# Optimization experiments

Measured on AMD Instinct MI355X. Metric: run time of the kernel, lower is better.

## Reference

```python
import jax, jax.numpy as jnp
import numpy as np

B, C, H = 8, 768, 12
TH = TW = 16
SH = SW = 32
N = TH * TW + SH * SW  # 1280


def setup_inputs() -> dict:
    key = jax.random.key(0)
    k1, k2, k3 = jax.random.split(key, 3)
    return {
        "x": jax.random.normal(k1, (B, N, C), jnp.float32),
        "qkv_w": jax.random.normal(k2, (3 * C, C), jnp.float32) * 0.02,
        "proj_w": jax.random.normal(k3, (C, C), jnp.float32) * 0.02,
        "proj_b": jnp.zeros((C,), jnp.float32),
        "t_h": TH, "t_w": TW, "s_h": SH, "s_w": SW,
    }


def reference(x, qkv_w, proj_w, proj_b, t_h, t_w, s_h, s_w):
    Bb, Nn, Cc = x.shape
    hd = Cc // H
    scale = hd ** -0.5
    nt = t_h * t_w
    ns = s_h * s_w
    # qkv projection: torch Linear computes x @ W.T
    qkv = (x @ qkv_w.T).reshape(Bb, Nn, 3, H, hd).transpose(2, 0, 3, 1, 4)
    q, k, v = qkv[0], qkv[1], qkv[2]  # each [B, H, N, hd]
    q_mt, q_s = q[:, :, :nt], q[:, :, nt:]
    k_mt, v_mt = k[:, :, :nt], v[:, :, :nt]
    # template queries attend only to template keys
    attn_t = jax.nn.softmax(jnp.einsum('bhqd,bhkd->bhqk', q_mt, k_mt) * scale, axis=-1)
    x_mt = jnp.einsum('bhqk,bhkd->bhqd', attn_t, v_mt).transpose(0, 2, 1, 3).reshape(Bb, nt, Cc)
    # search queries attend to all (template + search) keys
    attn_s = jax.nn.softmax(jnp.einsum('bhqd,bhkd->bhqk', q_s, k) * scale, axis=-1)
    x_s = jnp.einsum('bhqk,bhkd->bhqd', attn_s, v).transpose(0, 2, 1, 3).reshape(Bb, ns, Cc)
    out = jnp.concatenate([x_mt, x_s], axis=1)
    out = out @ proj_w.T + proj_b
    return out
```

## Files before the change

### kernel.cpp

```cpp
#include <hip/hip_runtime.h>


typedef __attribute__((ext_vector_type(8))) short s8v;
typedef __attribute__((ext_vector_type(4))) float f4v;
typedef __attribute__((ext_vector_type(4))) unsigned short u4v;

#define MFMA16(a, b, c) __builtin_amdgcn_mfma_f32_16x16x32_bf16((a), (b), (c), 0, 0, 0)

#define QSCALE 0.1803368801f

__device__ __forceinline__ unsigned short f2bf(float f) {
  unsigned int u = __builtin_bit_cast(unsigned int, f);
  u += 0x7fffu + ((u >> 16) & 1u);
  return (unsigned short)(u >> 16);
}

__global__ __launch_bounds__(256) void cvt_kernel(const float* __restrict__ src,
                                                  unsigned short* __restrict__ dst,
                                                  int n4) {
  int i = blockIdx.x * 256 + threadIdx.x;
  if (i < n4) {
    f4v v = ((const f4v*)src)[i];
    u4v o;
    o[0] = f2bf(v[0]); o[1] = f2bf(v[1]); o[2] = f2bf(v[2]); o[3] = f2bf(v[3]);
    ((u4v*)dst)[i] = o;
  }
}

__global__ __launch_bounds__(256) void gemm_qkv_kernel(
    const unsigned short* __restrict__ A,
    const unsigned short* __restrict__ Bm,
    unsigned short* __restrict__ qb, unsigned short* __restrict__ kb,
    unsigned short* __restrict__ vT) {
  const int K = 768;
  __shared__ __align__(16) unsigned short As[128 * 32];
  __shared__ __align__(16) unsigned short Bs[128 * 32];
  int tid = threadIdx.x;
  int wave = tid >> 6, lane = tid & 63;
  int quad = lane >> 4, l16 = lane & 15;
  int wm = wave >> 1, wn = wave & 1;
  int m0 = blockIdx.y * 128, n0 = blockIdx.x * 128;

  f4v acc[4][4];
#pragma unroll
  for (int i = 0; i < 4; ++i)
#pragma unroll
    for (int j = 0; j < 4; ++j) acc[i][j] = (f4v){0.f, 0.f, 0.f, 0.f};

  for (int kt = 0; kt < K; kt += 32) {
#pragma unroll
    for (int c = 0; c < 2; ++c) {
      int idx = c * 256 + tid;
      int row = idx >> 2;
      int col = (idx & 3) << 3;
      const unsigned short* ga = A + (size_t)(m0 + row) * K + (kt + col);
      const unsigned short* gb = Bm + (size_t)(n0 + row) * K + (kt + col);
      __builtin_amdgcn_global_load_lds(
          (const __attribute__((address_space(1))) unsigned int*)ga,
          (__attribute__((address_space(3))) unsigned int*)((char*)As + idx * 16), 16, 0, 0);
      __builtin_amdgcn_global_load_lds(
          (const __attribute__((address_space(1))) unsigned int*)gb,
          (__attribute__((address_space(3))) unsigned int*)((char*)Bs + idx * 16), 16, 0, 0);
    }
    __syncthreads();
    s8v af[4], bfr[4];
#pragma unroll
    for (int mi = 0; mi < 4; ++mi)
      af[mi] = *(const s8v*)&As[(wm * 64 + mi * 16 + l16) * 32 + quad * 8];
#pragma unroll
    for (int ni = 0; ni < 4; ++ni)
      bfr[ni] = *(const s8v*)&Bs[(wn * 64 + ni * 16 + l16) * 32 + quad * 8];
#pragma unroll
    for (int mi = 0; mi < 4; ++mi)
#pragma unroll
      for (int ni = 0; ni < 4; ++ni)
        acc[mi][ni] = MFMA16(af[mi], bfr[ni], acc[mi][ni]);
    __syncthreads();
  }

#pragma unroll
  for (int ni = 0; ni < 4; ++ni) {
    int gn = n0 + wn * 64 + ni * 16 + l16;
    int which = gn / 768;
    int oo = gn - which * 768;
    int hh = oo >> 6;
    int dd = oo & 63;
#pragma unroll
    for (int mi = 0; mi < 4; ++mi) {
#pragma unroll
      for (int r = 0; r < 4; ++r) {
        int gm = m0 + wm * 64 + mi * 16 + quad * 4 + r;
        int bb = gm / 1280;
        int nn = gm - bb * 1280;
        float v = acc[mi][ni][r];
        if (which == 0) {
          qb[(((size_t)bb * 12 + hh) * 1280 + nn) * 64 + dd] = f2bf(v * QSCALE);
        } else if (which == 1) {
          kb[(((size_t)bb * 12 + hh) * 1280 + nn) * 64 + dd] = f2bf(v);
        } else {
          vT[(((size_t)bb * 12 + hh) * 64 + dd) * 1280 + nn] = f2bf(v);
        }
      }
    }
  }
}

__global__ __launch_bounds__(256) void gemm_proj_kernel(
    const unsigned short* __restrict__ A,
    const unsigned short* __restrict__ Bm,
    const float* __restrict__ pb, float* __restrict__ out) {
  const int K = 768;
  __shared__ __align__(16) unsigned short As[128 * 32];
  __shared__ __align__(16) unsigned short Bs[128 * 32];
  int tid = threadIdx.x;
  int wave = tid >> 6, lane = tid & 63;
  int quad = lane >> 4, l16 = lane & 15;
  int wm = wave >> 1, wn = wave & 1;
  int m0 = blockIdx.y * 128, n0 = blockIdx.x * 128;

  f4v acc[4][4];
#pragma unroll
  for (int i = 0; i < 4; ++i)
#pragma unroll
    for (int j = 0; j < 4; ++j) acc[i][j] = (f4v){0.f, 0.f, 0.f, 0.f};

  for (int kt = 0; kt < K; kt += 32) {
#pragma unroll
    for (int c = 0; c < 2; ++c) {
      int idx = c * 256 + tid;
      int row = idx >> 2;
      int col = (idx & 3) << 3;
      const unsigned short* ga = A + (size_t)(m0 + row) * K + (kt + col);
      const unsigned short* gb = Bm + (size_t)(n0 + row) * K + (kt + col);
      __builtin_amdgcn_global_load_lds(
          (const __attribute__((address_space(1))) unsigned int*)ga,
          (__attribute__((address_space(3))) unsigned int*)((char*)As + idx * 16), 16, 0, 0);
      __builtin_amdgcn_global_load_lds(
          (const __attribute__((address_space(1))) unsigned int*)gb,
          (__attribute__((address_space(3))) unsigned int*)((char*)Bs + idx * 16), 16, 0, 0);
    }
    __syncthreads();
    s8v af[4], bfr[4];
#pragma unroll
    for (int mi = 0; mi < 4; ++mi)
      af[mi] = *(const s8v*)&As[(wm * 64 + mi * 16 + l16) * 32 + quad * 8];
#pragma unroll
    for (int ni = 0; ni < 4; ++ni)
      bfr[ni] = *(const s8v*)&Bs[(wn * 64 + ni * 16 + l16) * 32 + quad * 8];
#pragma unroll
    for (int mi = 0; mi < 4; ++mi)
#pragma unroll
      for (int ni = 0; ni < 4; ++ni)
        acc[mi][ni] = MFMA16(af[mi], bfr[ni], acc[mi][ni]);
    __syncthreads();
  }

#pragma unroll
  for (int ni = 0; ni < 4; ++ni) {
    int gn = n0 + wn * 64 + ni * 16 + l16;
    float bias = pb[gn];
#pragma unroll
    for (int mi = 0; mi < 4; ++mi)
#pragma unroll
      for (int r = 0; r < 4; ++r) {
        int gm = m0 + wm * 64 + mi * 16 + quad * 4 + r;
        out[(size_t)gm * 768 + gn] = acc[mi][ni][r] + bias;
      }
  }
}

__global__ __launch_bounds__(256) void attn_kernel(
    const unsigned short* __restrict__ qb, const unsigned short* __restrict__ kb,
    const unsigned short* __restrict__ vT, unsigned short* __restrict__ attnb) {
  const int NT = 1280, CC = 768;
  int bx = blockIdx.x;
  int qt = (bx < 16) ? (bx + 4) : (bx - 16);
  int h = blockIdx.y;
  int b = blockIdx.z;
  int wave = threadIdx.x >> 6, lane = threadIdx.x & 63;
  int quad = lane >> 4, l16 = lane & 15;
  int q0 = qt * 64 + wave * 16;
  int nk = (qt < 4) ? 256 : 1280;
  int ntiles = nk >> 6;

  const unsigned short* qp = qb + (((size_t)b * 12 + h) * NT + q0) * 64;
  const unsigned short* kp = kb + (((size_t)b * 12 + h) * NT) * 64;
  const unsigned short* vp = vT + (((size_t)b * 12 + h) * 64) * NT;

  __shared__ __align__(16) unsigned short Kl[2][8][512];
  __shared__ __align__(16) unsigned short Vl[2][8][512];

  s8v bq0 = *(const s8v*)(qp + l16 * 64 + quad * 8);
  s8v bq1 = *(const s8v*)(qp + l16 * 64 + 32 + quad * 8);

  int perm = ((l16 >> 2) << 3) + (l16 & 3);
  int f0 = wave * 2, f1 = wave * 2 + 1;
  int koffs0, koffs1, voffs0, voffs1;
  {
    int s = f0 >> 2, dh = (f0 >> 1) & 1, hh = f0 & 1;
    koffs0 = (s * 32 + hh * 4 + perm) * 64 + (dh * 4 + quad) * 8;
    s = f1 >> 2; dh = (f1 >> 1) & 1; hh = f1 & 1;
    koffs1 = (s * 32 + hh * 4 + perm) * 64 + (dh * 4 + quad) * 8;
    int dt = f0 >> 1, sv = f0 & 1;
    voffs0 = (dt * 16 + l16) * NT + sv * 32 + quad * 8;
    dt = f1 >> 1; sv = f1 & 1;
    voffs1 = (dt * 16 + l16) * NT + sv * 32 + quad * 8;
  }

#define STAGE(bfi, k0_)                                                                     \
  do {                                                                                      \
    __builtin_amdgcn_global_load_lds(                                                       \
        (const __attribute__((address_space(1))) unsigned int*)(kp + (size_t)(k0_)*64 +     \
                                                                koffs0),                    \
        (__attribute__((address_space(3))) unsigned int*)((char*)&Kl[bfi][f0][0] +          \
                                                          lane * 16),                       \
        16, 0, 0);                                                                          \
    __builtin_amdgcn_global_load_lds(                                                       \
        (const __attribute__((address_space(1))) unsigned int*)(kp + (size_t)(k0_)*64 +     \
                                                                koffs1),                    \
        (__attribute__((address_space(3))) unsigned int*)((char*)&Kl[bfi][f1][0] +          \
                                                          lane * 16),                       \
        16, 0, 0);                                                                          \
    __builtin_amdgcn_global_load_lds(                                                       \
        (const __attribute__((address_space(1))) unsigned int*)(vp + (size_t)(k0_) +        \
                                                                voffs0),                    \
        (__attribute__((address_space(3))) unsigned int*)((char*)&Vl[bfi][f0][0] +          \
                                                          lane * 16),                       \
        16, 0, 0);                                                                          \
    __builtin_amdgcn_global_load_lds(                                                       \
        (const __attribute__((address_space(1))) unsigned int*)(vp + (size_t)(k0_) +        \
                                                                voffs1),                    \
        (__attribute__((address_space(3))) unsigned int*)((char*)&Vl[bfi][f1][0] +          \
                                                          lane * 16),                       \
        16, 0, 0);                                                                          \
  } while (0)

  float l_part = 0.f;
  f4v Oacc[4];
#pragma unroll
  for (int dt = 0; dt < 4; ++dt) Oacc[dt] = (f4v){0.f, 0.f, 0.f, 0.f};

  STAGE(0, 0);

  for (int t = 0; t < ntiles; ++t) {
    __syncthreads();
    int bf = t & 1;
    if (t + 1 < ntiles) STAGE(bf ^ 1, (t + 1) * 64);

    s8v kf[8], vf[8];
#pragma unroll
    for (int f = 0; f < 8; ++f) kf[f] = *(const s8v*)&Kl[bf][f][lane * 8];
#pragma unroll
    for (int g = 0; g < 8; ++g) vf[g] = *(const s8v*)&Vl[bf][g][lane * 8];

#pragma unroll
    for (int s = 0; s < 2; ++s) {
      f4v s0 = {0.f, 0.f, 0.f, 0.f}, s1 = {0.f, 0.f, 0.f, 0.f};
      s0 = MFMA16(kf[(s << 2) | 0], bq0, s0);
      s0 = MFMA16(kf[(s << 2) | 2], bq1, s0);
      s1 = MFMA16(kf[(s << 2) | 1], bq0, s1);
      s1 = MFMA16(kf[(s << 2) | 3], bq1, s1);

      float p0[4], p1[4];
#pragma unroll
      for (int r = 0; r < 4; ++r) {
        p0[r] = __builtin_amdgcn_exp2f(s0[r]);
        p1[r] = __builtin_amdgcn_exp2f(s1[r]);
      }
      l_part += ((p0[0] + p0[1]) + (p0[2] + p0[3])) + ((p1[0] + p1[1]) + (p1[2] + p1[3]));

      s8v pbf;
#pragma unroll
      for (int r = 0; r < 4; ++r) {
        pbf[r] = (short)f2bf(p0[r]);
        pbf[4 + r] = (short)f2bf(p1[r]);
      }

#pragma unroll
      for (int dt = 0; dt < 4; ++dt) Oacc[dt] = MFMA16(vf[dt * 2 + s], pbf, Oacc[dt]);
    }
  }
#undef STAGE

  float l = l_part;
  l += __shfl_xor(l, 16, 64);
  l += __shfl_xor(l, 32, 64);
  float inv = 1.f / l;

  size_t orow = ((size_t)b * NT + q0 + l16) * CC + h * 64;
#pragma unroll
  for (int dt = 0; dt < 4; ++dt) {
    u4v ov;
#pragma unroll
    for (int r = 0; r < 4; ++r) ov[r] = f2bf(Oacc[dt][r] * inv);
    *(u4v*)(attnb + orow + dt * 16 + quad * 4) = ov;
  }
}

extern "C" void kernel_launch(void* const* d_in, const int* in_sizes, int n_in,
                              void* d_out, int out_size, void* d_ws, size_t ws_size,
                              hipStream_t stream) {
  const float* x = (const float*)d_in[0];
  const float* qkv_w = (const float*)d_in[1];
  const float* proj_w = (const float*)d_in[2];
  const float* proj_b = (const float*)d_in[3];
  float* out = (float*)d_out;

  char* ws = (char*)d_ws;
  unsigned short* xb = (unsigned short*)(ws + 0);
  unsigned short* wqkvb = (unsigned short*)(ws + 15728640);
  unsigned short* wpb = (unsigned short*)(ws + 19267584);
  unsigned short* qb = (unsigned short*)(ws + 20447232);
  unsigned short* kbuf = (unsigned short*)(ws + 36175872);
  unsigned short* vT = (unsigned short*)(ws + 51904512);
  unsigned short* attnb = xb;

  cvt_kernel<<<dim3(1966080 / 256), 256, 0, stream>>>(x, xb, 1966080);
  cvt_kernel<<<dim3(442368 / 256), 256, 0, stream>>>(qkv_w, wqkvb, 442368);
  cvt_kernel<<<dim3(576), 256, 0, stream>>>(proj_w, wpb, 147456);

  gemm_qkv_kernel<<<dim3(18, 80), 256, 0, stream>>>(xb, wqkvb, qb, kbuf, vT);
  attn_kernel<<<dim3(20, 12, 8), 256, 0, stream>>>(qb, kbuf, vT, attnb);
  gemm_proj_kernel<<<dim3(6, 80), 256, 0, stream>>>(attnb, wpb, proj_b, out);
}
```

Measured before the change: 285.2 us.

## Process 32 queries per wave in attention to reuse K/V tiles; fuse conversions

Each attention wave now handles two 16-row query blocks (128 queries per block), so every K/V fragment loaded from LDS feeds twice as many MFMAs and the grid is halved. The probability packing uses the packed bf16 conversion intrinsic, and the three fp32-to-bf16 conversion launches become one kernel. In exchange, register pressure per wave rises and there are fewer blocks to keep the GPU busy.

```diff
diff --git a/kernel.cpp b/kernel.cpp
--- a/kernel.cpp
+++ b/kernel.cpp
@@ -1,9 +1,11 @@
 #include <hip/hip_runtime.h>
+#include <hip/hip_bf16.h>
 
 
 typedef __attribute__((ext_vector_type(8))) short s8v;
 typedef __attribute__((ext_vector_type(4))) float f4v;
 typedef __attribute__((ext_vector_type(4))) unsigned short u4v;
+typedef __attribute__((ext_vector_type(4))) unsigned int u4i;
 
 #define MFMA16(a, b, c) __builtin_amdgcn_mfma_f32_16x16x32_bf16((a), (b), (c), 0, 0, 0)
 
@@ -15,16 +17,43 @@
   return (unsigned short)(u >> 16);
 }
 
-__global__ __launch_bounds__(256) void cvt_kernel(const float* __restrict__ src,
-                                                  unsigned short* __restrict__ dst,
-                                                  int n4) {
+__device__ __forceinline__ unsigned int pk2(float lo, float hi) {
+  __hip_bfloat162 t = __float22bfloat162_rn(make_float2(lo, hi));
+  unsigned int u;
+  __builtin_memcpy(&u, &t, 4);
+  return u;
+}
+
+__device__ __forceinline__ s8v pack8(const float* p0, const float* p1) {
+  u4i pi;
+  pi[0] = pk2(p0[0], p0[1]);
+  pi[1] = pk2(p0[2], p0[3]);
+  pi[2] = pk2(p1[0], p1[1]);
+  pi[3] = pk2(p1[2], p1[3]);
+  return __builtin_bit_cast(s8v, pi);
+}
+
+__global__ __launch_bounds__(256) void cvt3_kernel(const float* __restrict__ x,
+                                                   const float* __restrict__ wq,
+                                                   const float* __restrict__ wp,
+                                                   unsigned short* __restrict__ xb,
+                                                   unsigned short* __restrict__ wqb,
+                                                   unsigned short* __restrict__ wpb) {
   int i = blockIdx.x * 256 + threadIdx.x;
-  if (i < n4) {
-    f4v v = ((const f4v*)src)[i];
-    u4v o;
-    o[0] = f2bf(v[0]); o[1] = f2bf(v[1]); o[2] = f2bf(v[2]); o[3] = f2bf(v[3]);
-    ((u4v*)dst)[i] = o;
-  }
+  const float* src;
+  unsigned short* dst;
+  int j;
+  if (i < 1966080) {
+    src = x; dst = xb; j = i;
+  } else if (i < 1966080 + 442368) {
+    src = wq; dst = wqb; j = i - 1966080;
+  } else {
+    src = wp; dst = wpb; j = i - (1966080 + 442368);
+  }
+  f4v v = ((const f4v*)src)[j];
+  u4v o;
+  o[0] = f2bf(v[0]); o[1] = f2bf(v[1]); o[2] = f2bf(v[2]); o[3] = f2bf(v[3]);
+  ((u4v*)dst)[j] = o;
 }
 
 __global__ __launch_bounds__(256) void gemm_qkv_kernel(
@@ -174,16 +203,17 @@
     const unsigned short* __restrict__ vT, unsigned short* __restrict__ attnb) {
   const int NT = 1280, CC = 768;
   int bx = blockIdx.x;
-  int qt = (bx < 16) ? (bx + 4) : (bx - 16);
   int h = blockIdx.y;
   int b = blockIdx.z;
+  int nk, qstart;
+  if (bx < 8) { nk = 1280; qstart = 256 + bx * 128; }
+  else        { nk = 256;  qstart = (bx - 8) * 128; }
   int wave = threadIdx.x >> 6, lane = threadIdx.x & 63;
   int quad = lane >> 4, l16 = lane & 15;
-  int q0 = qt * 64 + wave * 16;
-  int nk = (qt < 4) ? 256 : 1280;
+  int qa = qstart + wave * 32;
   int ntiles = nk >> 6;
 
-  const unsigned short* qp = qb + (((size_t)b * 12 + h) * NT + q0) * 64;
+  const unsigned short* qp = qb + (((size_t)b * 12 + h) * NT + qa) * 64;
   const unsigned short* kp = kb + (((size_t)b * 12 + h) * NT) * 64;
   const unsigned short* vp = vT + (((size_t)b * 12 + h) * 64) * NT;
 
@@ -192,6 +222,8 @@
 
   s8v bq0 = *(const s8v*)(qp + l16 * 64 + quad * 8);
   s8v bq1 = *(const s8v*)(qp + l16 * 64 + 32 + quad * 8);
+  s8v bq2 = *(const s8v*)(qp + (16 + l16) * 64 + quad * 8);
+  s8v bq3 = *(const s8v*)(qp + (16 + l16) * 64 + 32 + quad * 8);
 
   int perm = ((l16 >> 2) << 3) + (l16 & 3);
   int f0 = wave * 2, f1 = wave * 2 + 1;
@@ -235,10 +267,13 @@
         16, 0, 0);                                                                          \
   } while (0)
 
-  float l_part = 0.f;
-  f4v Oacc[4];
-#pragma unroll
-  for (int dt = 0; dt < 4; ++dt) Oacc[dt] = (f4v){0.f, 0.f, 0.f, 0.f};
+  float la = 0.f, lb = 0.f;
+  f4v Oa[4], Ob[4];
+#pragma unroll
+  for (int dt = 0; dt < 4; ++dt) {
+    Oa[dt] = (f4v){0.f, 0.f, 0.f, 0.f};
+    Ob[dt] = (f4v){0.f, 0.f, 0.f, 0.f};
+  }
 
   STAGE(0, 0);
 
@@ -255,45 +290,59 @@
 
 #pragma unroll
     for (int s = 0; s < 2; ++s) {
-      f4v s0 = {0.f, 0.f, 0.f, 0.f}, s1 = {0.f, 0.f, 0.f, 0.f};
-      s0 = MFMA16(kf[(s << 2) | 0], bq0, s0);
-      s0 = MFMA16(kf[(s << 2) | 2], bq1, s0);
-      s1 = MFMA16(kf[(s << 2) | 1], bq0, s1);
-      s1 = MFMA16(kf[(s << 2) | 3], bq1, s1);
-
-      float p0[4], p1[4];
+      int s4 = s << 2;
+      f4v s0a = {0.f, 0.f, 0.f, 0.f}, s1a = {0.f, 0.f, 0.f, 0.f};
+      f4v s0b = {0.f, 0.f, 0.f, 0.f}, s1b = {0.f, 0.f, 0.f, 0.f};
+      s0a = MFMA16(kf[s4 | 0], bq0, s0a);
+      s0a = MFMA16(kf[s4 | 2], bq1, s0a);
+      s1a = MFMA16(kf[s4 | 1], bq0, s1a);
+      s1a = MFMA16(kf[s4 | 3], bq1, s1a);
+      s0b = MFMA16(kf[s4 | 0], bq2, s0b);
+      s0b = MFMA16(kf[s4 | 2], bq3, s0b);
+      s1b = MFMA16(kf[s4 | 1], bq2, s1b);
+      s1b = MFMA16(kf[s4 | 3], bq3, s1b);
+
+      float p0a[4], p1a[4], p0b[4], p1b[4];
 #pragma unroll
       for (int r = 0; r < 4; ++r) {
-        p0[r] = __builtin_amdgcn_exp2f(s0[r]);
-        p1[r] = __builtin_amdgcn_exp2f(s1[r]);
+        p0a[r] = __builtin_amdgcn_exp2f(s0a[r]);
+        p1a[r] = __builtin_amdgcn_exp2f(s1a[r]);
+        p0b[r] = __builtin_amdgcn_exp2f(s0b[r]);
+        p1b[r] = __builtin_amdgcn_exp2f(s1b[r]);
       }
-      l_part += ((p0[0] + p0[1]) + (p0[2] + p0[3])) + ((p1[0] + p1[1]) + (p1[2] + p1[3]));
-
-      s8v pbf;
-#pragma unroll
-      for (int r = 0; r < 4; ++r) {
-        pbf[r] = (short)f2bf(p0[r]);
-        pbf[4 + r] = (short)f2bf(p1[r]);
+      la += ((p0a[0] + p0a[1]) + (p0a[2] + p0a[3])) + ((p1a[0] + p1a[1]) + (p1a[2] + p1a[3]));
+      lb += ((p0b[0] + p0b[1]) + (p0b[2] + p0b[3])) + ((p1b[0] + p1b[1]) + (p1b[2] + p1b[3]));
+
+      s8v pa = pack8(p0a, p1a);
+      s8v pbv = pack8(p0b, p1b);
+
+#pragma unroll
+      for (int dt = 0; dt < 4; ++dt) {
+        Oa[dt] = MFMA16(vf[dt * 2 + s], pa, Oa[dt]);
+        Ob[dt] = MFMA16(vf[dt * 2 + s], pbv, Ob[dt]);
       }
-
-#pragma unroll
-      for (int dt = 0; dt < 4; ++dt) Oacc[dt] = MFMA16(vf[dt * 2 + s], pbf, Oacc[dt]);
     }
   }
 #undef STAGE
 
-  float l = l_part;
-  l += __shfl_xor(l, 16, 64);
-  l += __shfl_xor(l, 32, 64);
-  float inv = 1.f / l;
-
-  size_t orow = ((size_t)b * NT + q0 + l16) * CC + h * 64;
+  la += __shfl_xor(la, 16, 64);
+  la += __shfl_xor(la, 32, 64);
+  lb += __shfl_xor(lb, 16, 64);
+  lb += __shfl_xor(lb, 32, 64);
+  float inva = 1.f / la, invb = 1.f / lb;
+
+  size_t rowa = ((size_t)b * NT + qa + l16) * CC + h * 64;
+  size_t rowb = ((size_t)b * NT + qa + 16 + l16) * CC + h * 64;
 #pragma unroll
   for (int dt = 0; dt < 4; ++dt) {
-    u4v ov;
-#pragma unroll
-    for (int r = 0; r < 4; ++r) ov[r] = f2bf(Oacc[dt][r] * inv);
-    *(u4v*)(attnb + orow + dt * 16 + quad * 4) = ov;
+    u4v ova, ovb;
+#pragma unroll
+    for (int r = 0; r < 4; ++r) {
+      ova[r] = f2bf(Oa[dt][r] * inva);
+      ovb[r] = f2bf(Ob[dt][r] * invb);
+    }
+    *(u4v*)(attnb + rowa + dt * 16 + quad * 4) = ova;
+    *(u4v*)(attnb + rowb + dt * 16 + quad * 4) = ovb;
   }
 }
 
@@ -315,11 +364,9 @@
   unsigned short* vT = (unsigned short*)(ws + 51904512);
   unsigned short* attnb = xb;
 
-  cvt_kernel<<<dim3(1966080 / 256), 256, 0, stream>>>(x, xb, 1966080);
-  cvt_kernel<<<dim3(442368 / 256), 256, 0, stream>>>(qkv_w, wqkvb, 442368);
-  cvt_kernel<<<dim3(576), 256, 0, stream>>>(proj_w, wpb, 147456);
+  cvt3_kernel<<<dim3(9984), 256, 0, stream>>>(x, qkv_w, proj_w, xb, wqkvb, wpb);
 
   gemm_qkv_kernel<<<dim3(18, 80), 256, 0, stream>>>(xb, wqkvb, qb, kbuf, vT);
-  attn_kernel<<<dim3(20, 12, 8), 256, 0, stream>>>(qb, kbuf, vT, attnb);
+  attn_kernel<<<dim3(10, 12, 8), 256, 0, stream>>>(qb, kbuf, vT, attnb);
   gemm_proj_kernel<<<dim3(6, 80), 256, 0, stream>>>(attnb, wpb, proj_b, out);
 }
```

Measured after the change: 280.1 us. Within noise of the previous version (-1.8%).
